# Performance work log

Hardware: AMD Instinct MI355X
Metric: run time of the kernel (lower is better)

The kernel has to match this reference:

```python
import jax, jax.numpy as jnp
import numpy as np

N = 50000        # nodes
E = 1600000      # edges (before self loops)
IN = 256         # in_channels
C = 32           # hidden_channels (per head)
H = 4            # heads
OUT = 64         # out_channels
NEG_SLOPE = 0.2  # PyG GATConv default


def setup_inputs() -> dict:
    key = jax.random.key(0)
    ks = jax.random.split(key, 8)
    x = jax.random.normal(ks[0], (N, IN), dtype=jnp.float32)
    edge_index = jax.random.randint(ks[1], (2, E), 0, N, dtype=jnp.int64)
    s = 0.05
    W = jax.random.normal(ks[2], (IN, H * C), dtype=jnp.float32) * s
    att_src = jax.random.normal(ks[3], (H, C), dtype=jnp.float32) * s
    att_dst = jax.random.normal(ks[4], (H, C), dtype=jnp.float32) * s
    bias = jnp.zeros((H * C,), dtype=jnp.float32)
    lin_W = jax.random.normal(ks[5], (H * C, OUT), dtype=jnp.float32) * s
    lin_b = jnp.zeros((OUT,), dtype=jnp.float32)
    return {"x": x, "edge_index": edge_index, "W": W, "att_src": att_src,
            "att_dst": att_dst, "bias": bias, "lin_W": lin_W, "lin_b": lin_b}


def reference(x, edge_index, W, att_src, att_dst, bias, lin_W, lin_b):
    # Linear transform per head: [N, H, C]
    h = (x @ W).reshape(N, H, C)
    # Per-node attention halves (PyG GATConv): [N, H]
    a_src = jnp.einsum('nhc,hc->nh', h, att_src)
    a_dst = jnp.einsum('nhc,hc->nh', h, att_dst)
    # Add self loops (PyG default add_self_loops=True)
    loop = jnp.arange(N, dtype=edge_index.dtype)
    src = jnp.concatenate([edge_index[0], loop])  # message source j
    dst = jnp.concatenate([edge_index[1], loop])  # message target i
    # Edge attention logits: LeakyReLU(a_src[j] + a_dst[i])  -> [E+N, H]
    e = jax.nn.leaky_relu(a_src[src] + a_dst[dst], negative_slope=NEG_SLOPE)
    # Segment softmax over incoming edges of each destination node
    emax = jax.lax.stop_gradient(jax.ops.segment_max(e, dst, num_segments=N))
    emax = jnp.where(jnp.isfinite(emax), emax, 0.0)
    ex = jnp.exp(e - emax[dst])
    denom = jax.ops.segment_sum(ex, dst, num_segments=N)
    alpha = ex / denom[dst]  # [E+N, H]; self loops guarantee denom > 0
    # Weighted scatter-sum of source features: [N, H, C]
    msg = alpha[:, :, None] * h[src]
    agg = jax.ops.segment_sum(msg, dst, num_segments=N)
    out = agg.reshape(N, H * C) + bias  # concat heads + bias
    out = jax.nn.elu(out)
    return out @ lin_W + lin_b
```

## Files before the change

### kernel.cpp

```cpp
#include <hip/hip_runtime.h>
#include <cstdint>
#include <cstddef>

#define N_NODES 50000
#define N_EDGES 1600000
#define TOT_E   (N_EDGES + N_NODES)
#define IN_DIM  256
#define HC      128
#define NHEAD   4
#define OUT_DIM 64

#define SHIFT   7
#define BSZ     128
#define NBUK    ((N_NODES + BSZ - 1) / BSZ)
#define CHUNK   2048
#define EPT     8
#define NCHUNK  ((TOT_E + CHUNK - 1) / CHUNK)
#define NREP    8
#define CAPR    768
#define CAP     (NREP * CAPR)
#define STRIDE  88
#define ROWW    (STRIDE / 2)

#define K1_ROWS 32
#define XPAD 264
#define HPAD 132
#define K1_NB ((N_NODES + K1_ROWS - 1) / K1_ROWS)

#define W2_GEMM_BLK ((HC * IN_DIM) / 256)
#define W2_LIN_BLK  ((OUT_DIM * HC) / 256)

typedef __attribute__((ext_vector_type(8))) short bf16x8;
typedef __attribute__((ext_vector_type(4))) float f32x4;
typedef __attribute__((ext_vector_type(4))) unsigned short u16x4;

static __device__ __forceinline__ uint16_t f2bf(float f) {
    uint32_t u = __float_as_uint(f);
    uint32_t r = (u + 0x7fffu + ((u >> 16) & 1u)) >> 16;
    return (uint16_t)r;
}
static __device__ __forceinline__ float bf_lo(uint32_t u) {
    return __uint_as_float(u << 16);
}
static __device__ __forceinline__ float bf_hi(uint32_t u) {
    return __uint_as_float(u & 0xffff0000u);
}

__global__ __launch_bounds__(256) void w2bf(const float* __restrict__ W,
                                            const float* __restrict__ linW,
                                            uint16_t* __restrict__ wt,
                                            uint16_t* __restrict__ lwt,
                                            int* __restrict__ gcur) {
    if (blockIdx.x < W2_GEMM_BLK) {
        int idx = blockIdx.x * 256 + threadIdx.x;
        int n = idx >> 8, k = idx & 255;
        wt[idx] = f2bf(W[(size_t)k * HC + n]);
        if (idx < NBUK * NREP) gcur[idx] = 0;
    } else {
        int idx = (blockIdx.x - W2_GEMM_BLK) * 256 + threadIdx.x;
        int n = idx >> 7, k = idx & 127;
        float w = linW[(size_t)k * OUT_DIM + n];
        uint16_t h = f2bf(w);
        float hf = __uint_as_float((uint32_t)h << 16);
        lwt[idx] = h;
        lwt[OUT_DIM * HC + idx] = f2bf(w - hf);
    }
}

__global__ __launch_bounds__(256) void k1p3(const float* __restrict__ x,
                                            const uint16_t* __restrict__ wt,
                                            const float* __restrict__ att_src,
                                            const float* __restrict__ att_dst,
                                            uint16_t* __restrict__ hb,
                                            float* __restrict__ a_src,
                                            float* __restrict__ a_dst,
                                            const int* __restrict__ ei,
                                            int* __restrict__ gcur,
                                            uint32_t* __restrict__ binned) {
    __shared__ char smem[K1_ROWS * 528];
    __shared__ float att_s[HC], att_d[HC];
    const int tid = threadIdx.x;

    if (blockIdx.x < K1_NB) {
        uint16_t* xs = (uint16_t*)smem;
        float*    hs = (float*)smem;
        const int wave = tid >> 6;
        const int lane = tid & 63;
        const int m    = lane & 15;
        const int q    = lane >> 4;
        const int row0 = blockIdx.x * K1_ROWS;
        const int wr   = (wave >> 1) * 16;
        const int wc   = (wave & 1) * 64;

        if (tid < HC) { att_s[tid] = att_src[tid]; att_d[tid] = att_dst[tid]; }

        for (int i = tid * 4; i < K1_ROWS * IN_DIM; i += 1024) {
            int r = i >> 8, c = i & 255;
            int gr = row0 + r;
            float4 v = make_float4(0.f, 0.f, 0.f, 0.f);
            if (gr < N_NODES) v = *(const float4*)(x + (size_t)gr * IN_DIM + c);
            uint32_t lo = (uint32_t)f2bf(v.x) | ((uint32_t)f2bf(v.y) << 16);
            uint32_t hi = (uint32_t)f2bf(v.z) | ((uint32_t)f2bf(v.w) << 16);
            *(uint2*)(xs + r * XPAD + c) = make_uint2(lo, hi);
        }
        __syncthreads();

        f32x4 acc[4];
        #pragma unroll
        for (int t = 0; t < 4; ++t) acc[t] = (f32x4){0.f, 0.f, 0.f, 0.f};

        const int arow = wr + m;
        #pragma unroll
        for (int ks = 0; ks < IN_DIM; ks += 32) {
            bf16x8 a = *(const bf16x8*)(xs + arow * XPAD + ks + q * 8);
            #pragma unroll
            for (int t = 0; t < 4; ++t) {
                bf16x8 b = *(const bf16x8*)(wt + (size_t)(wc + t * 16 + m) * IN_DIM + ks + q * 8);
                acc[t] = __builtin_amdgcn_mfma_f32_16x16x32_bf16(a, b, acc[t], 0, 0, 0);
            }
        }
        __syncthreads();

        #pragma unroll
        for (int t = 0; t < 4; ++t)
            #pragma unroll
            for (int r = 0; r < 4; ++r)
                hs[(wr + q * 4 + r) * HPAD + wc + t * 16 + m] = acc[t][r];
        __syncthreads();

        for (int i = tid * 4; i < K1_ROWS * HC; i += 1024) {
            int r = i >> 7, c = i & 127;
            if (row0 + r < N_NODES) {
                float4 v = *(const float4*)(hs + r * HPAD + c);
                uint32_t lo = (uint32_t)f2bf(v.x) | ((uint32_t)f2bf(v.y) << 16);
                uint32_t hi = (uint32_t)f2bf(v.z) | ((uint32_t)f2bf(v.w) << 16);
                *(uint2*)(hb + (size_t)(row0 + r) * HC + c) = make_uint2(lo, hi);
            }
        }
        if (tid < K1_ROWS * NHEAD) {
            int r = tid >> 2, hd = tid & 3;
            if (row0 + r < N_NODES) {
                float s = 0.f, d = 0.f;
                #pragma unroll
                for (int j = 0; j < 32; ++j) {
                    float v = hs[r * HPAD + hd * 32 + j];
                    s = fmaf(v, att_s[hd * 32 + j], s);
                    d = fmaf(v, att_d[hd * 32 + j], d);
                }
                a_src[(row0 + r) * NHEAD + hd] = s;
                a_dst[(row0 + r) * NHEAD + hd] = d;
            }
        }
    } else {
        int* hist = (int*)smem;
        int* lcur = hist + NBUK;
        for (int i = tid; i < NBUK; i += 256) hist[i] = 0;
        __syncthreads();

        uint32_t wreg[EPT];
        const int pblk = blockIdx.x - K1_NB;
        const int rep  = pblk & (NREP - 1);
        const int base = pblk * CHUNK;
        #pragma unroll
        for (int k = 0; k < EPT; ++k) {
            int e = base + k * 256 + tid;
            uint32_t word = 0xFFFFFFFFu;
            if (e < TOT_E) {
                int src, dst;
                if (e < N_EDGES) { src = ei[e]; dst = ei[N_EDGES + e]; }
                else             { src = e - N_EDGES; dst = src; }
                int b = dst >> SHIFT;
                word = (uint32_t)src | ((uint32_t)(dst & (BSZ - 1)) << 16)
                     | ((uint32_t)b << 23);
                atomicAdd(&hist[b], 1);
            }
            wreg[k] = word;
        }
        __syncthreads();
        for (int i = tid; i < NBUK; i += 256) {
            int c = hist[i];
            lcur[i] = c ? atomicAdd(&gcur[rep * NBUK + i], c) : 0;
        }
        __syncthreads();
        #pragma unroll
        for (int k = 0; k < EPT; ++k) {
            uint32_t word = wreg[k];
            if (word != 0xFFFFFFFFu) {
                int b = (int)(word >> 23);
                int pos = atomicAdd(&lcur[b], 1);
                if (pos < CAPR)
                    binned[(size_t)b * CAP + rep * CAPR + pos] = word;
            }
        }
    }
}

__global__ __launch_bounds__(256) void rgrp(const uint32_t* __restrict__ binned,
                                            const int* __restrict__ gcur,
                                            uint16_t* __restrict__ csr,
                                            int* __restrict__ cnt) {
    __shared__ uint32_t lcsr32[BSZ * ROWW];
    __shared__ int ncnt[BSZ];
    const int b   = blockIdx.x;
    const int tid = threadIdx.x;

    for (int j = tid; j < BSZ * ROWW; j += 256) lcsr32[j] = 0;
    if (tid < BSZ) ncnt[tid] = 0;
    __syncthreads();

    uint16_t* lcsr16 = (uint16_t*)lcsr32;
    #pragma unroll
    for (int rep = 0; rep < NREP; ++rep) {
        int c = gcur[rep * NBUK + b];
        if (c > CAPR) c = CAPR;
        const uint32_t* bb = binned + (size_t)b * CAP + rep * CAPR;
        for (int i = tid; i < c; i += 256) {
            uint32_t w = bb[i];
            int dl  = (w >> 16) & (BSZ - 1);
            int pos = atomicAdd(&ncnt[dl], 1);
            if (pos < STRIDE) lcsr16[dl * STRIDE + pos] = (uint16_t)(w & 0xFFFFu);
        }
    }
    __syncthreads();

    const int node0 = b * BSZ;
    uint32_t* csr32 = (uint32_t*)csr;
    for (int j = tid; j < BSZ * ROWW; j += 256) {
        int r = j / ROWW, w = j - r * ROWW;
        int node = node0 + r;
        if (node < N_NODES)
            csr32[(size_t)node * ROWW + w] = lcsr32[j];
    }
    if (tid < BSZ && node0 + tid < N_NODES) cnt[node0 + tid] = ncnt[tid];
}

__global__ __launch_bounds__(512, 6) void q4_agg(const uint16_t* __restrict__ csr,
                                                 const int* __restrict__ cnt,
                                                 const uint32_t* __restrict__ hb32,
                                                 const float* __restrict__ a_src,
                                                 const float* __restrict__ a_dst,
                                                 const float* __restrict__ bias,
                                                 uint32_t* __restrict__ actb) {
    const int tid  = threadIdx.x;
    const int wave = tid >> 6;
    const int lane = tid & 63;
    const int g    = lane >> 4;
    const int sl   = lane & 15;
    const int head = sl >> 2;
    const int baseln = g << 4;
    const char*  hb8 = (const char*)hb32 + sl * 16;
    const float* ash = a_src + head;
    const float4 bA = *(const float4*)(bias + sl * 8);
    const float4 bB = *(const float4*)(bias + sl * 8 + 4);

    const int node = blockIdx.x * 32 + wave * 4 + g;
    int myc = 0;
    if (node < N_NODES) myc = min(cnt[node], STRIDE);
    const uint16_t* crow = csr + (size_t)min(node, N_NODES - 1) * STRIDE;

    int m1   = max(myc, __shfl_xor(myc, 16, 64));
    int maxc = max(m1,  __shfl_xor(m1, 32, 64));
    const int nit = (maxc + 3) >> 2;
    const float ad = a_dst[min(node, N_NODES - 1) * NHEAD + head];

    uint2 svq = *(const uint2*)(crow + sl * 4);
    const int svlo = (int)svq.x, svhi = (int)svq.y;

    float l = 0.f;
    float acc[8];
    #pragma unroll
    for (int j = 0; j < 8; ++j) acc[j] = 0.f;

    uint4 ph0 = make_uint4(0, 0, 0, 0), ph1 = ph0, ph2 = ph0, ph3 = ph0;
    float pa0 = 0.f, pa1 = 0.f, pa2 = 0.f, pa3 = 0.f;
    if (nit > 0) {
        uint32_t lo = (uint32_t)__shfl(svlo, baseln, 64);
        uint32_t hi = (uint32_t)__shfl(svhi, baseln, 64);
        int s0 = (int)(lo & 0xFFFFu), s1 = (int)(lo >> 16);
        int s2 = (int)(hi & 0xFFFFu), s3 = (int)(hi >> 16);
        pa0 = ash[s0 * NHEAD];
        pa1 = ash[s1 * NHEAD];
        pa2 = ash[s2 * NHEAD];
        pa3 = ash[s3 * NHEAD];
        ph0 = *(const uint4*)(hb8 + ((uint32_t)s0 << 8));
        ph1 = *(const uint4*)(hb8 + ((uint32_t)s1 << 8));
        ph2 = *(const uint4*)(hb8 + ((uint32_t)s2 << 8));
        ph3 = *(const uint4*)(hb8 + ((uint32_t)s3 << 8));
    }

    for (int it = 0; it < nit; ++it) {
        const int i = it * 4;
        const uint4 h0 = ph0, h1 = ph1, h2 = ph2, h3 = ph3;
        const float as0 = pa0, as1 = pa1, as2 = pa2, as3 = pa3;
        if (it + 1 < nit) {
            int s0, s1, s2, s3;
            if (it + 1 < 16) {
                uint32_t lo = (uint32_t)__shfl(svlo, baseln + it + 1, 64);
                uint32_t hi = (uint32_t)__shfl(svhi, baseln + it + 1, 64);
                s0 = (int)(lo & 0xFFFFu); s1 = (int)(lo >> 16);
                s2 = (int)(hi & 0xFFFFu); s3 = (int)(hi >> 16);
            } else {
                u16x4 nv = *(const u16x4*)(crow + i + 4);
                s0 = nv[0]; s1 = nv[1]; s2 = nv[2]; s3 = nv[3];
            }
            pa0 = ash[s0 * NHEAD];
            pa1 = ash[s1 * NHEAD];
            pa2 = ash[s2 * NHEAD];
            pa3 = ash[s3 * NHEAD];
            ph0 = *(const uint4*)(hb8 + ((uint32_t)s0 << 8));
            ph1 = *(const uint4*)(hb8 + ((uint32_t)s1 << 8));
            ph2 = *(const uint4*)(hb8 + ((uint32_t)s2 << 8));
            ph3 = *(const uint4*)(hb8 + ((uint32_t)s3 << 8));
        }

        float e0 = as0 + ad, e1 = as1 + ad, e2 = as2 + ad, e3 = as3 + ad;
        e0 = fmaxf(e0, 0.2f * e0);
        e1 = fmaxf(e1, 0.2f * e1);
        e2 = fmaxf(e2, 0.2f * e2);
        e3 = fmaxf(e3, 0.2f * e3);
        float w0 = __expf(e0), w1 = __expf(e1);
        float w2 = __expf(e2), w3 = __expf(e3);
        w0 = (i + 0 < myc) ? w0 : 0.f;
        w1 = (i + 1 < myc) ? w1 : 0.f;
        w2 = (i + 2 < myc) ? w2 : 0.f;
        w3 = (i + 3 < myc) ? w3 : 0.f;
        l += (w0 + w1) + (w2 + w3);
        acc[0] = fmaf(w0, bf_lo(h0.x), acc[0]); acc[0] = fmaf(w1, bf_lo(h1.x), acc[0]);
        acc[0] = fmaf(w2, bf_lo(h2.x), acc[0]); acc[0] = fmaf(w3, bf_lo(h3.x), acc[0]);
        acc[1] = fmaf(w0, bf_hi(h0.x), acc[1]); acc[1] = fmaf(w1, bf_hi(h1.x), acc[1]);
        acc[1] = fmaf(w2, bf_hi(h2.x), acc[1]); acc[1] = fmaf(w3, bf_hi(h3.x), acc[1]);
        acc[2] = fmaf(w0, bf_lo(h0.y), acc[2]); acc[2] = fmaf(w1, bf_lo(h1.y), acc[2]);
        acc[2] = fmaf(w2, bf_lo(h2.y), acc[2]); acc[2] = fmaf(w3, bf_lo(h3.y), acc[2]);
        acc[3] = fmaf(w0, bf_hi(h0.y), acc[3]); acc[3] = fmaf(w1, bf_hi(h1.y), acc[3]);
        acc[3] = fmaf(w2, bf_hi(h2.y), acc[3]); acc[3] = fmaf(w3, bf_hi(h3.y), acc[3]);
        acc[4] = fmaf(w0, bf_lo(h0.z), acc[4]); acc[4] = fmaf(w1, bf_lo(h1.z), acc[4]);
        acc[4] = fmaf(w2, bf_lo(h2.z), acc[4]); acc[4] = fmaf(w3, bf_lo(h3.z), acc[4]);
        acc[5] = fmaf(w0, bf_hi(h0.z), acc[5]); acc[5] = fmaf(w1, bf_hi(h1.z), acc[5]);
        acc[5] = fmaf(w2, bf_hi(h2.z), acc[5]); acc[5] = fmaf(w3, bf_hi(h3.z), acc[5]);
        acc[6] = fmaf(w0, bf_lo(h0.w), acc[6]); acc[6] = fmaf(w1, bf_lo(h1.w), acc[6]);
        acc[6] = fmaf(w2, bf_lo(h2.w), acc[6]); acc[6] = fmaf(w3, bf_lo(h3.w), acc[6]);
        acc[7] = fmaf(w0, bf_hi(h0.w), acc[7]); acc[7] = fmaf(w1, bf_hi(h1.w), acc[7]);
        acc[7] = fmaf(w2, bf_hi(h2.w), acc[7]); acc[7] = fmaf(w3, bf_hi(h3.w), acc[7]);
    }

    if (node < N_NODES) {
        const float inv = 1.f / l;
        float o[8];
        o[0] = fmaf(acc[0], inv, bA.x); o[1] = fmaf(acc[1], inv, bA.y);
        o[2] = fmaf(acc[2], inv, bA.z); o[3] = fmaf(acc[3], inv, bA.w);
        o[4] = fmaf(acc[4], inv, bB.x); o[5] = fmaf(acc[5], inv, bB.y);
        o[6] = fmaf(acc[6], inv, bB.z); o[7] = fmaf(acc[7], inv, bB.w);
        #pragma unroll
        for (int j = 0; j < 8; ++j)
            o[j] = (o[j] > 0.f) ? o[j] : (__expf(o[j]) - 1.f);
        uint4 pk;
        pk.x = (uint32_t)f2bf(o[0]) | ((uint32_t)f2bf(o[1]) << 16);
        pk.y = (uint32_t)f2bf(o[2]) | ((uint32_t)f2bf(o[3]) << 16);
        pk.z = (uint32_t)f2bf(o[4]) | ((uint32_t)f2bf(o[5]) << 16);
        pk.w = (uint32_t)f2bf(o[6]) | ((uint32_t)f2bf(o[7]) << 16);
        *(uint4*)(actb + (size_t)node * 64 + sl * 4) = pk;
    }
}

__global__ __launch_bounds__(256) void k7_out(const uint16_t* __restrict__ ab,
                                              const uint16_t* __restrict__ lwt,
                                              const float* __restrict__ linb,
                                              float* __restrict__ out) {
    __shared__ uint16_t as_[64][136];
    const int tid  = threadIdx.x;
    const int row0 = blockIdx.x * 64;

    for (int i = tid; i < 64 * 16; i += 256) {
        int r = i >> 4, cw = i & 15;
        int node = row0 + r;
        uint4 v = make_uint4(0, 0, 0, 0);
        if (node < N_NODES) v = *(const uint4*)(ab + (size_t)node * HC + cw * 8);
        *(uint4*)(&as_[r][cw * 8]) = v;
    }
    __syncthreads();

    const int wave = tid >> 6;
    const int lane = tid & 63;
    const int m    = lane & 15;
    const int q    = lane >> 4;
    const uint16_t* lwlo = lwt + OUT_DIM * HC;

    f32x4 acc[4];
    #pragma unroll
    for (int t = 0; t < 4; ++t) acc[t] = (f32x4){0.f, 0.f, 0.f, 0.f};

    const int arow = wave * 16 + m;
    #pragma unroll
    for (int ks = 0; ks < HC; ks += 32) {
        bf16x8 a = *(const bf16x8*)(&as_[arow][ks + q * 8]);
        #pragma unroll
        for (int t = 0; t < 4; ++t) {
            bf16x8 bh = *(const bf16x8*)(lwt  + (size_t)(t * 16 + m) * HC + ks + q * 8);
            bf16x8 bl = *(const bf16x8*)(lwlo + (size_t)(t * 16 + m) * HC + ks + q * 8);
            acc[t] = __builtin_amdgcn_mfma_f32_16x16x32_bf16(a, bh, acc[t], 0, 0, 0);
            acc[t] = __builtin_amdgcn_mfma_f32_16x16x32_bf16(a, bl, acc[t], 0, 0, 0);
        }
    }

    const int grow = row0 + wave * 16 + q * 4;
    #pragma unroll
    for (int t = 0; t < 4; ++t) {
        const int col = t * 16 + m;
        const float lb = linb[col];
        #pragma unroll
        for (int r = 0; r < 4; ++r)
            if (grow + r < N_NODES)
                out[(size_t)(grow + r) * OUT_DIM + col] = acc[t][r] + lb;
    }
}

extern "C" void kernel_launch(void* const* d_in, const int* in_sizes, int n_in,
                              void* d_out, int out_size, void* d_ws, size_t ws_size,
                              hipStream_t stream) {
    (void)in_sizes; (void)n_in; (void)out_size; (void)ws_size;
    const float* x       = (const float*)d_in[0];
    const int*   ei      = (const int*)d_in[1];
    const float* W       = (const float*)d_in[2];
    const float* att_src = (const float*)d_in[3];
    const float* att_dst = (const float*)d_in[4];
    const float* bias    = (const float*)d_in[5];
    const float* linW    = (const float*)d_in[6];
    const float* linb    = (const float*)d_in[7];
    float*       out     = (float*)d_out;

    char*  ws  = (char*)d_ws;
    size_t off = 0;
    auto alloc = [&](size_t bytes) -> void* {
        void* p = ws + off;
        off += (bytes + 255) & ~(size_t)255;
        return p;
    };
    uint16_t* hb     = (uint16_t*)alloc((size_t)N_NODES * HC * 2);
    uint16_t* wt     = (uint16_t*)alloc((size_t)HC * IN_DIM * 2);
    uint32_t* actb   = (uint32_t*)alloc((size_t)N_NODES * 64 * 4);
    float*    a_src  = (float*)alloc((size_t)N_NODES * NHEAD * 4);
    float*    a_dst  = (float*)alloc((size_t)N_NODES * NHEAD * 4);
    int*      gcur   = (int*)alloc((size_t)NBUK * NREP * 4);
    uint32_t* binned = (uint32_t*)alloc((size_t)NBUK * CAP * 4);
    int*      cnt    = (int*)alloc((size_t)N_NODES * 4);
    uint16_t* csr    = (uint16_t*)alloc((size_t)N_NODES * STRIDE * 2);
    uint16_t* lwt    = (uint16_t*)alloc((size_t)2 * OUT_DIM * HC * 2);

    w2bf<<<W2_GEMM_BLK + W2_LIN_BLK, 256, 0, stream>>>(W, linW, wt, lwt, gcur);
    k1p3<<<K1_NB + NCHUNK, 256, 0, stream>>>(x, wt, att_src, att_dst,
                                             hb, a_src, a_dst,
                                             ei, gcur, binned);
    rgrp<<<NBUK, 256, 0, stream>>>(binned, gcur, csr, cnt);
    q4_agg<<<(N_NODES + 31) / 32, 512, 0, stream>>>(csr, cnt, (const uint32_t*)hb,
                                                    a_src, a_dst, bias, actb);
    k7_out<<<(N_NODES + 63) / 64, 256, 0, stream>>>((const uint16_t*)actb, lwt,
                                                    linb, out);
}
```

Before: 225.5 us.

## Fuse CSR regrouping into aggregation kernel using shared-memory adjacency

```diff
diff --git a/kernel.cpp b/kernel.cpp
--- a/kernel.cpp
+++ b/kernel.cpp
@@ -195,53 +195,40 @@
     }
 }
 
-__global__ __launch_bounds__(256) void rgrp(const uint32_t* __restrict__ binned,
-                                            const int* __restrict__ gcur,
-                                            uint16_t* __restrict__ csr,
-                                            int* __restrict__ cnt) {
-    __shared__ uint32_t lcsr32[BSZ * ROWW];
-    __shared__ int ncnt[BSZ];
-    const int b   = blockIdx.x;
-    const int tid = threadIdx.x;
-
-    for (int j = tid; j < BSZ * ROWW; j += 256) lcsr32[j] = 0;
-    if (tid < BSZ) ncnt[tid] = 0;
+__global__ __launch_bounds__(512, 6) void q4_agg(const uint32_t* __restrict__ binned,
+                                                 const int* __restrict__ gcur,
+                                                 const uint32_t* __restrict__ hb32,
+                                                 const float* __restrict__ a_src,
+                                                 const float* __restrict__ a_dst,
+                                                 const float* __restrict__ bias,
+                                                 uint32_t* __restrict__ actb) {
+    __shared__ uint16_t lcsr[64 * STRIDE];
+    __shared__ int ncnt[64];
+    const int b    = blockIdx.x >> 1;
+    const int half = blockIdx.x & 1;
+    const int tid  = threadIdx.x;
+
+    for (int j = tid; j < 64 * ROWW; j += 512) ((uint32_t*)lcsr)[j] = 0;
+    if (tid < 64) ncnt[tid] = 0;
     __syncthreads();
 
-    uint16_t* lcsr16 = (uint16_t*)lcsr32;
     #pragma unroll
     for (int rep = 0; rep < NREP; ++rep) {
         int c = gcur[rep * NBUK + b];
         if (c > CAPR) c = CAPR;
         const uint32_t* bb = binned + (size_t)b * CAP + rep * CAPR;
-        for (int i = tid; i < c; i += 256) {
+        for (int i = tid; i < c; i += 512) {
             uint32_t w = bb[i];
-            int dl  = (w >> 16) & (BSZ - 1);
-            int pos = atomicAdd(&ncnt[dl], 1);
-            if (pos < STRIDE) lcsr16[dl * STRIDE + pos] = (uint16_t)(w & 0xFFFFu);
+            int dl = (w >> 16) & (BSZ - 1);
+            if ((dl >> 6) == half) {
+                int ln  = dl & 63;
+                int pos = atomicAdd(&ncnt[ln], 1);
+                if (pos < STRIDE) lcsr[ln * STRIDE + pos] = (uint16_t)(w & 0xFFFFu);
+            }
         }
     }
     __syncthreads();
 
-    const int node0 = b * BSZ;
-    uint32_t* csr32 = (uint32_t*)csr;
-    for (int j = tid; j < BSZ * ROWW; j += 256) {
-        int r = j / ROWW, w = j - r * ROWW;
-        int node = node0 + r;
-        if (node < N_NODES)
-            csr32[(size_t)node * ROWW + w] = lcsr32[j];
-    }
-    if (tid < BSZ && node0 + tid < N_NODES) cnt[node0 + tid] = ncnt[tid];
-}
-
-__global__ __launch_bounds__(512, 6) void q4_agg(const uint16_t* __restrict__ csr,
-                                                 const int* __restrict__ cnt,
-                                                 const uint32_t* __restrict__ hb32,
-                                                 const float* __restrict__ a_src,
-                                                 const float* __restrict__ a_dst,
-                                                 const float* __restrict__ bias,
-                                                 uint32_t* __restrict__ actb) {
-    const int tid  = threadIdx.x;
     const int wave = tid >> 6;
     const int lane = tid & 63;
     const int g    = lane >> 4;
@@ -253,56 +240,33 @@
     const float4 bA = *(const float4*)(bias + sl * 8);
     const float4 bB = *(const float4*)(bias + sl * 8 + 4);
 
-    const int node = blockIdx.x * 32 + wave * 4 + g;
-    int myc = 0;
-    if (node < N_NODES) myc = min(cnt[node], STRIDE);
-    const uint16_t* crow = csr + (size_t)min(node, N_NODES - 1) * STRIDE;
-
-    int m1   = max(myc, __shfl_xor(myc, 16, 64));
-    int maxc = max(m1,  __shfl_xor(m1, 32, 64));
-    const int nit = (maxc + 3) >> 2;
-    const float ad = a_dst[min(node, N_NODES - 1) * NHEAD + head];
-
-    uint2 svq = *(const uint2*)(crow + sl * 4);
-    const int svlo = (int)svq.x, svhi = (int)svq.y;
-
-    float l = 0.f;
-    float acc[8];
-    #pragma unroll
-    for (int j = 0; j < 8; ++j) acc[j] = 0.f;
-
-    uint4 ph0 = make_uint4(0, 0, 0, 0), ph1 = ph0, ph2 = ph0, ph3 = ph0;
-    float pa0 = 0.f, pa1 = 0.f, pa2 = 0.f, pa3 = 0.f;
-    if (nit > 0) {
-        uint32_t lo = (uint32_t)__shfl(svlo, baseln, 64);
-        uint32_t hi = (uint32_t)__shfl(svhi, baseln, 64);
-        int s0 = (int)(lo & 0xFFFFu), s1 = (int)(lo >> 16);
-        int s2 = (int)(hi & 0xFFFFu), s3 = (int)(hi >> 16);
-        pa0 = ash[s0 * NHEAD];
-        pa1 = ash[s1 * NHEAD];
-        pa2 = ash[s2 * NHEAD];
-        pa3 = ash[s3 * NHEAD];
-        ph0 = *(const uint4*)(hb8 + ((uint32_t)s0 << 8));
-        ph1 = *(const uint4*)(hb8 + ((uint32_t)s1 << 8));
-        ph2 = *(const uint4*)(hb8 + ((uint32_t)s2 << 8));
-        ph3 = *(const uint4*)(hb8 + ((uint32_t)s3 << 8));
-    }
-
-    for (int it = 0; it < nit; ++it) {
-        const int i = it * 4;
-        const uint4 h0 = ph0, h1 = ph1, h2 = ph2, h3 = ph3;
-        const float as0 = pa0, as1 = pa1, as2 = pa2, as3 = pa3;
-        if (it + 1 < nit) {
-            int s0, s1, s2, s3;
-            if (it + 1 < 16) {
-                uint32_t lo = (uint32_t)__shfl(svlo, baseln + it + 1, 64);
-                uint32_t hi = (uint32_t)__shfl(svhi, baseln + it + 1, 64);
-                s0 = (int)(lo & 0xFFFFu); s1 = (int)(lo >> 16);
-                s2 = (int)(hi & 0xFFFFu); s3 = (int)(hi >> 16);
-            } else {
-                u16x4 nv = *(const u16x4*)(crow + i + 4);
-                s0 = nv[0]; s1 = nv[1]; s2 = nv[2]; s3 = nv[3];
-            }
+    for (int pass = 0; pass < 2; ++pass) {
+        const int ln   = pass * 32 + wave * 4 + g;
+        const int node = b * BSZ + half * 64 + ln;
+        int myc = 0;
+        if (node < N_NODES) myc = min(ncnt[ln], STRIDE);
+        const uint16_t* crow = lcsr + ln * STRIDE;
+
+        int m1   = max(myc, __shfl_xor(myc, 16, 64));
+        int maxc = max(m1,  __shfl_xor(m1, 32, 64));
+        const int nit = (maxc + 3) >> 2;
+        const float ad = a_dst[min(node, N_NODES - 1) * NHEAD + head];
+
+        uint2 svq = *(const uint2*)(crow + sl * 4);
+        const int svlo = (int)svq.x, svhi = (int)svq.y;
+
+        float l = 0.f;
+        float acc[8];
+        #pragma unroll
+        for (int j = 0; j < 8; ++j) acc[j] = 0.f;
+
+        uint4 ph0 = make_uint4(0, 0, 0, 0), ph1 = ph0, ph2 = ph0, ph3 = ph0;
+        float pa0 = 0.f, pa1 = 0.f, pa2 = 0.f, pa3 = 0.f;
+        if (nit > 0) {
+            uint32_t lo = (uint32_t)__shfl(svlo, baseln, 64);
+            uint32_t hi = (uint32_t)__shfl(svhi, baseln, 64);
+            int s0 = (int)(lo & 0xFFFFu), s1 = (int)(lo >> 16);
+            int s2 = (int)(hi & 0xFFFFu), s3 = (int)(hi >> 16);
             pa0 = ash[s0 * NHEAD];
             pa1 = ash[s1 * NHEAD];
             pa2 = ash[s2 * NHEAD];
@@ -313,52 +277,78 @@
             ph3 = *(const uint4*)(hb8 + ((uint32_t)s3 << 8));
         }
 
-        float e0 = as0 + ad, e1 = as1 + ad, e2 = as2 + ad, e3 = as3 + ad;
-        e0 = fmaxf(e0, 0.2f * e0);
-        e1 = fmaxf(e1, 0.2f * e1);
-        e2 = fmaxf(e2, 0.2f * e2);
-        e3 = fmaxf(e3, 0.2f * e3);
-        float w0 = __expf(e0), w1 = __expf(e1);
-        float w2 = __expf(e2), w3 = __expf(e3);
-        w0 = (i + 0 < myc) ? w0 : 0.f;
-        w1 = (i + 1 < myc) ? w1 : 0.f;
-        w2 = (i + 2 < myc) ? w2 : 0.f;
-        w3 = (i + 3 < myc) ? w3 : 0.f;
-        l += (w0 + w1) + (w2 + w3);
-        acc[0] = fmaf(w0, bf_lo(h0.x), acc[0]); acc[0] = fmaf(w1, bf_lo(h1.x), acc[0]);
-        acc[0] = fmaf(w2, bf_lo(h2.x), acc[0]); acc[0] = fmaf(w3, bf_lo(h3.x), acc[0]);
-        acc[1] = fmaf(w0, bf_hi(h0.x), acc[1]); acc[1] = fmaf(w1, bf_hi(h1.x), acc[1]);
-        acc[1] = fmaf(w2, bf_hi(h2.x), acc[1]); acc[1] = fmaf(w3, bf_hi(h3.x), acc[1]);
-        acc[2] = fmaf(w0, bf_lo(h0.y), acc[2]); acc[2] = fmaf(w1, bf_lo(h1.y), acc[2]);
-        acc[2] = fmaf(w2, bf_lo(h2.y), acc[2]); acc[2] = fmaf(w3, bf_lo(h3.y), acc[2]);
-        acc[3] = fmaf(w0, bf_hi(h0.y), acc[3]); acc[3] = fmaf(w1, bf_hi(h1.y), acc[3]);
-        acc[3] = fmaf(w2, bf_hi(h2.y), acc[3]); acc[3] = fmaf(w3, bf_hi(h3.y), acc[3]);
-        acc[4] = fmaf(w0, bf_lo(h0.z), acc[4]); acc[4] = fmaf(w1, bf_lo(h1.z), acc[4]);
-        acc[4] = fmaf(w2, bf_lo(h2.z), acc[4]); acc[4] = fmaf(w3, bf_lo(h3.z), acc[4]);
-        acc[5] = fmaf(w0, bf_hi(h0.z), acc[5]); acc[5] = fmaf(w1, bf_hi(h1.z), acc[5]);
-        acc[5] = fmaf(w2, bf_hi(h2.z), acc[5]); acc[5] = fmaf(w3, bf_hi(h3.z), acc[5]);
-        acc[6] = fmaf(w0, bf_lo(h0.w), acc[6]); acc[6] = fmaf(w1, bf_lo(h1.w), acc[6]);
-        acc[6] = fmaf(w2, bf_lo(h2.w), acc[6]); acc[6] = fmaf(w3, bf_lo(h3.w), acc[6]);
-        acc[7] = fmaf(w0, bf_hi(h0.w), acc[7]); acc[7] = fmaf(w1, bf_hi(h1.w), acc[7]);
-        acc[7] = fmaf(w2, bf_hi(h2.w), acc[7]); acc[7] = fmaf(w3, bf_hi(h3.w), acc[7]);
-    }
-
-    if (node < N_NODES) {
-        const float inv = 1.f / l;
-        float o[8];
-        o[0] = fmaf(acc[0], inv, bA.x); o[1] = fmaf(acc[1], inv, bA.y);
-        o[2] = fmaf(acc[2], inv, bA.z); o[3] = fmaf(acc[3], inv, bA.w);
-        o[4] = fmaf(acc[4], inv, bB.x); o[5] = fmaf(acc[5], inv, bB.y);
-        o[6] = fmaf(acc[6], inv, bB.z); o[7] = fmaf(acc[7], inv, bB.w);
-        #pragma unroll
-        for (int j = 0; j < 8; ++j)
-            o[j] = (o[j] > 0.f) ? o[j] : (__expf(o[j]) - 1.f);
-        uint4 pk;
-        pk.x = (uint32_t)f2bf(o[0]) | ((uint32_t)f2bf(o[1]) << 16);
-        pk.y = (uint32_t)f2bf(o[2]) | ((uint32_t)f2bf(o[3]) << 16);
-        pk.z = (uint32_t)f2bf(o[4]) | ((uint32_t)f2bf(o[5]) << 16);
-        pk.w = (uint32_t)f2bf(o[6]) | ((uint32_t)f2bf(o[7]) << 16);
-        *(uint4*)(actb + (size_t)node * 64 + sl * 4) = pk;
+        for (int it = 0; it < nit; ++it) {
+            const int i = it * 4;
+            const uint4 h0 = ph0, h1 = ph1, h2 = ph2, h3 = ph3;
+            const float as0 = pa0, as1 = pa1, as2 = pa2, as3 = pa3;
+            if (it + 1 < nit) {
+                int s0, s1, s2, s3;
+                if (it + 1 < 16) {
+                    uint32_t lo = (uint32_t)__shfl(svlo, baseln + it + 1, 64);
+                    uint32_t hi = (uint32_t)__shfl(svhi, baseln + it + 1, 64);
+                    s0 = (int)(lo & 0xFFFFu); s1 = (int)(lo >> 16);
+                    s2 = (int)(hi & 0xFFFFu); s3 = (int)(hi >> 16);
+                } else {
+                    u16x4 nv = *(const u16x4*)(crow + i + 4);
+                    s0 = nv[0]; s1 = nv[1]; s2 = nv[2]; s3 = nv[3];
+                }
+                pa0 = ash[s0 * NHEAD];
+                pa1 = ash[s1 * NHEAD];
+                pa2 = ash[s2 * NHEAD];
+                pa3 = ash[s3 * NHEAD];
+                ph0 = *(const uint4*)(hb8 + ((uint32_t)s0 << 8));
+                ph1 = *(const uint4*)(hb8 + ((uint32_t)s1 << 8));
+                ph2 = *(const uint4*)(hb8 + ((uint32_t)s2 << 8));
+                ph3 = *(const uint4*)(hb8 + ((uint32_t)s3 << 8));
+            }
+
+            float e0 = as0 + ad, e1 = as1 + ad, e2 = as2 + ad, e3 = as3 + ad;
+            e0 = fmaxf(e0, 0.2f * e0);
+            e1 = fmaxf(e1, 0.2f * e1);
+            e2 = fmaxf(e2, 0.2f * e2);
+            e3 = fmaxf(e3, 0.2f * e3);
+            float w0 = __expf(e0), w1 = __expf(e1);
+            float w2 = __expf(e2), w3 = __expf(e3);
+            w0 = (i + 0 < myc) ? w0 : 0.f;
+            w1 = (i + 1 < myc) ? w1 : 0.f;
+            w2 = (i + 2 < myc) ? w2 : 0.f;
+            w3 = (i + 3 < myc) ? w3 : 0.f;
+            l += (w0 + w1) + (w2 + w3);
+            acc[0] = fmaf(w0, bf_lo(h0.x), acc[0]); acc[0] = fmaf(w1, bf_lo(h1.x), acc[0]);
+            acc[0] = fmaf(w2, bf_lo(h2.x), acc[0]); acc[0] = fmaf(w3, bf_lo(h3.x), acc[0]);
+            acc[1] = fmaf(w0, bf_hi(h0.x), acc[1]); acc[1] = fmaf(w1, bf_hi(h1.x), acc[1]);
+            acc[1] = fmaf(w2, bf_hi(h2.x), acc[1]); acc[1] = fmaf(w3, bf_hi(h3.x), acc[1]);
+            acc[2] = fmaf(w0, bf_lo(h0.y), acc[2]); acc[2] = fmaf(w1, bf_lo(h1.y), acc[2]);
+            acc[2] = fmaf(w2, bf_lo(h2.y), acc[2]); acc[2] = fmaf(w3, bf_lo(h3.y), acc[2]);
+            acc[3] = fmaf(w0, bf_hi(h0.y), acc[3]); acc[3] = fmaf(w1, bf_hi(h1.y), acc[3]);
+            acc[3] = fmaf(w2, bf_hi(h2.y), acc[3]); acc[3] = fmaf(w3, bf_hi(h3.y), acc[3]);
+            acc[4] = fmaf(w0, bf_lo(h0.z), acc[4]); acc[4] = fmaf(w1, bf_lo(h1.z), acc[4]);
+            acc[4] = fmaf(w2, bf_lo(h2.z), acc[4]); acc[4] = fmaf(w3, bf_lo(h3.z), acc[4]);
+            acc[5] = fmaf(w0, bf_hi(h0.z), acc[5]); acc[5] = fmaf(w1, bf_hi(h1.z), acc[5]);
+            acc[5] = fmaf(w2, bf_hi(h2.z), acc[5]); acc[5] = fmaf(w3, bf_hi(h3.z), acc[5]);
+            acc[6] = fmaf(w0, bf_lo(h0.w), acc[6]); acc[6] = fmaf(w1, bf_lo(h1.w), acc[6]);
+            acc[6] = fmaf(w2, bf_lo(h2.w), acc[6]); acc[6] = fmaf(w3, bf_lo(h3.w), acc[6]);
+            acc[7] = fmaf(w0, bf_hi(h0.w), acc[7]); acc[7] = fmaf(w1, bf_hi(h1.w), acc[7]);
+            acc[7] = fmaf(w2, bf_hi(h2.w), acc[7]); acc[7] = fmaf(w3, bf_hi(h3.w), acc[7]);
+        }
+
+        if (node < N_NODES) {
+            const float inv = 1.f / l;
+            float o[8];
+            o[0] = fmaf(acc[0], inv, bA.x); o[1] = fmaf(acc[1], inv, bA.y);
+            o[2] = fmaf(acc[2], inv, bA.z); o[3] = fmaf(acc[3], inv, bA.w);
+            o[4] = fmaf(acc[4], inv, bB.x); o[5] = fmaf(acc[5], inv, bB.y);
+            o[6] = fmaf(acc[6], inv, bB.z); o[7] = fmaf(acc[7], inv, bB.w);
+            #pragma unroll
+            for (int j = 0; j < 8; ++j)
+                o[j] = (o[j] > 0.f) ? o[j] : (__expf(o[j]) - 1.f);
+            uint4 pk;
+            pk.x = (uint32_t)f2bf(o[0]) | ((uint32_t)f2bf(o[1]) << 16);
+            pk.y = (uint32_t)f2bf(o[2]) | ((uint32_t)f2bf(o[3]) << 16);
+            pk.z = (uint32_t)f2bf(o[4]) | ((uint32_t)f2bf(o[5]) << 16);
+            pk.w = (uint32_t)f2bf(o[6]) | ((uint32_t)f2bf(o[7]) << 16);
+            *(uint4*)(actb + (size_t)node * 64 + sl * 4) = pk;
+        }
     }
 }
 
@@ -442,17 +432,14 @@
     float*    a_dst  = (float*)alloc((size_t)N_NODES * NHEAD * 4);
     int*      gcur   = (int*)alloc((size_t)NBUK * NREP * 4);
     uint32_t* binned = (uint32_t*)alloc((size_t)NBUK * CAP * 4);
-    int*      cnt    = (int*)alloc((size_t)N_NODES * 4);
-    uint16_t* csr    = (uint16_t*)alloc((size_t)N_NODES * STRIDE * 2);
     uint16_t* lwt    = (uint16_t*)alloc((size_t)2 * OUT_DIM * HC * 2);
 
     w2bf<<<W2_GEMM_BLK + W2_LIN_BLK, 256, 0, stream>>>(W, linW, wt, lwt, gcur);
     k1p3<<<K1_NB + NCHUNK, 256, 0, stream>>>(x, wt, att_src, att_dst,
                                              hb, a_src, a_dst,
                                              ei, gcur, binned);
-    rgrp<<<NBUK, 256, 0, stream>>>(binned, gcur, csr, cnt);
-    q4_agg<<<(N_NODES + 31) / 32, 512, 0, stream>>>(csr, cnt, (const uint32_t*)hb,
-                                                    a_src, a_dst, bias, actb);
+    q4_agg<<<NBUK * 2, 512, 0, stream>>>(binned, gcur, (const uint32_t*)hb,
+                                         a_src, a_dst, bias, actb);
     k7_out<<<(N_NODES + 63) / 64, 256, 0, stream>>>((const uint16_t*)actb, lwt,
                                                     linb, out);
 }
```

Result: no change. 227.2 us (+0.8%).

## Fuse output linear layer into aggregation kernel via shared-memory MFMA epilogue

Applied to the files above, without the earlier changes.

```diff
diff --git a/kernel.cpp b/kernel.cpp
--- a/kernel.cpp
+++ b/kernel.cpp
@@ -234,13 +234,16 @@
     if (tid < BSZ && node0 + tid < N_NODES) cnt[node0 + tid] = ncnt[tid];
 }
 
-__global__ __launch_bounds__(512, 6) void q4_agg(const uint16_t* __restrict__ csr,
-                                                 const int* __restrict__ cnt,
-                                                 const uint32_t* __restrict__ hb32,
-                                                 const float* __restrict__ a_src,
-                                                 const float* __restrict__ a_dst,
-                                                 const float* __restrict__ bias,
-                                                 uint32_t* __restrict__ actb) {
+__global__ __launch_bounds__(512, 6) void q4k7(const uint16_t* __restrict__ csr,
+                                               const int* __restrict__ cnt,
+                                               const uint32_t* __restrict__ hb32,
+                                               const float* __restrict__ a_src,
+                                               const float* __restrict__ a_dst,
+                                               const float* __restrict__ bias,
+                                               const uint16_t* __restrict__ lwt,
+                                               const float* __restrict__ linb,
+                                               float* __restrict__ out) {
+    __shared__ uint16_t as_[32][136];
     const int tid  = threadIdx.x;
     const int wave = tid >> 6;
     const int lane = tid & 63;
@@ -253,7 +256,8 @@
     const float4 bA = *(const float4*)(bias + sl * 8);
     const float4 bB = *(const float4*)(bias + sl * 8 + 4);
 
-    const int node = blockIdx.x * 32 + wave * 4 + g;
+    const int ln   = wave * 4 + g;
+    const int node = blockIdx.x * 32 + ln;
     int myc = 0;
     if (node < N_NODES) myc = min(cnt[node], STRIDE);
     const uint16_t* crow = csr + (size_t)min(node, N_NODES - 1) * STRIDE;
@@ -343,6 +347,7 @@
         acc[7] = fmaf(w2, bf_hi(h2.w), acc[7]); acc[7] = fmaf(w3, bf_hi(h3.w), acc[7]);
     }
 
+    uint4 pk = make_uint4(0, 0, 0, 0);
     if (node < N_NODES) {
         const float inv = 1.f / l;
         float o[8];
@@ -353,65 +358,38 @@
         #pragma unroll
         for (int j = 0; j < 8; ++j)
             o[j] = (o[j] > 0.f) ? o[j] : (__expf(o[j]) - 1.f);
-        uint4 pk;
         pk.x = (uint32_t)f2bf(o[0]) | ((uint32_t)f2bf(o[1]) << 16);
         pk.y = (uint32_t)f2bf(o[2]) | ((uint32_t)f2bf(o[3]) << 16);
         pk.z = (uint32_t)f2bf(o[4]) | ((uint32_t)f2bf(o[5]) << 16);
         pk.w = (uint32_t)f2bf(o[6]) | ((uint32_t)f2bf(o[7]) << 16);
-        *(uint4*)(actb + (size_t)node * 64 + sl * 4) = pk;
-    }
-}
-
-__global__ __launch_bounds__(256) void k7_out(const uint16_t* __restrict__ ab,
-                                              const uint16_t* __restrict__ lwt,
-                                              const float* __restrict__ linb,
-                                              float* __restrict__ out) {
-    __shared__ uint16_t as_[64][136];
-    const int tid  = threadIdx.x;
-    const int row0 = blockIdx.x * 64;
-
-    for (int i = tid; i < 64 * 16; i += 256) {
-        int r = i >> 4, cw = i & 15;
-        int node = row0 + r;
-        uint4 v = make_uint4(0, 0, 0, 0);
-        if (node < N_NODES) v = *(const uint4*)(ab + (size_t)node * HC + cw * 8);
-        *(uint4*)(&as_[r][cw * 8]) = v;
-    }
+    }
+    *(uint4*)(&as_[ln][sl * 8]) = pk;
     __syncthreads();
 
-    const int wave = tid >> 6;
-    const int lane = tid & 63;
-    const int m    = lane & 15;
-    const int q    = lane >> 4;
+    const int m   = lane & 15;
+    const int q   = lane >> 4;
+    const int wr  = (wave >> 2) * 16;
+    const int wcl = (wave & 3) * 16;
     const uint16_t* lwlo = lwt + OUT_DIM * HC;
 
-    f32x4 acc[4];
-    #pragma unroll
-    for (int t = 0; t < 4; ++t) acc[t] = (f32x4){0.f, 0.f, 0.f, 0.f};
-
-    const int arow = wave * 16 + m;
+    f32x4 oacc = (f32x4){0.f, 0.f, 0.f, 0.f};
+    const int arow = wr + m;
     #pragma unroll
     for (int ks = 0; ks < HC; ks += 32) {
         bf16x8 a = *(const bf16x8*)(&as_[arow][ks + q * 8]);
-        #pragma unroll
-        for (int t = 0; t < 4; ++t) {
-            bf16x8 bh = *(const bf16x8*)(lwt  + (size_t)(t * 16 + m) * HC + ks + q * 8);
-            bf16x8 bl = *(const bf16x8*)(lwlo + (size_t)(t * 16 + m) * HC + ks + q * 8);
-            acc[t] = __builtin_amdgcn_mfma_f32_16x16x32_bf16(a, bh, acc[t], 0, 0, 0);
-            acc[t] = __builtin_amdgcn_mfma_f32_16x16x32_bf16(a, bl, acc[t], 0, 0, 0);
-        }
-    }
-
-    const int grow = row0 + wave * 16 + q * 4;
+        bf16x8 bh = *(const bf16x8*)(lwt  + (size_t)(wcl + m) * HC + ks + q * 8);
+        bf16x8 bl = *(const bf16x8*)(lwlo + (size_t)(wcl + m) * HC + ks + q * 8);
+        oacc = __builtin_amdgcn_mfma_f32_16x16x32_bf16(a, bh, oacc, 0, 0, 0);
+        oacc = __builtin_amdgcn_mfma_f32_16x16x32_bf16(a, bl, oacc, 0, 0, 0);
+    }
+
+    const int col  = wcl + m;
+    const float lb = linb[col];
+    const int grow = blockIdx.x * 32 + wr + q * 4;
     #pragma unroll
-    for (int t = 0; t < 4; ++t) {
-        const int col = t * 16 + m;
-        const float lb = linb[col];
-        #pragma unroll
-        for (int r = 0; r < 4; ++r)
-            if (grow + r < N_NODES)
-                out[(size_t)(grow + r) * OUT_DIM + col] = acc[t][r] + lb;
-    }
+    for (int r = 0; r < 4; ++r)
+        if (grow + r < N_NODES)
+            out[(size_t)(grow + r) * OUT_DIM + col] = oacc[r] + lb;
 }
 
 extern "C" void kernel_launch(void* const* d_in, const int* in_sizes, int n_in,
@@ -437,7 +415,6 @@
     };
     uint16_t* hb     = (uint16_t*)alloc((size_t)N_NODES * HC * 2);
     uint16_t* wt     = (uint16_t*)alloc((size_t)HC * IN_DIM * 2);
-    uint32_t* actb   = (uint32_t*)alloc((size_t)N_NODES * 64 * 4);
     float*    a_src  = (float*)alloc((size_t)N_NODES * NHEAD * 4);
     float*    a_dst  = (float*)alloc((size_t)N_NODES * NHEAD * 4);
     int*      gcur   = (int*)alloc((size_t)NBUK * NREP * 4);
@@ -451,8 +428,7 @@
                                              hb, a_src, a_dst,
                                              ei, gcur, binned);
     rgrp<<<NBUK, 256, 0, stream>>>(binned, gcur, csr, cnt);
-    q4_agg<<<(N_NODES + 31) / 32, 512, 0, stream>>>(csr, cnt, (const uint32_t*)hb,
-                                                    a_src, a_dst, bias, actb);
-    k7_out<<<(N_NODES + 63) / 64, 256, 0, stream>>>((const uint16_t*)actb, lwt,
-                                                    linb, out);
-}
+    q4k7<<<(N_NODES + 31) / 32, 512, 0, stream>>>(csr, cnt, (const uint32_t*)hb,
+                                                  a_src, a_dst, bias,
+                                                  lwt, linb, out);
+}
```

Result: faster. 214.8 us (median of 2 runs) (-4.7%).
